# Performance work log

Hardware: AMD Instinct MI355X
Metric: run time of the kernel (lower is better)

The kernel has to match this reference:

```python
import jax, jax.numpy as jnp
import numpy as np

N_NODES = 100000
N_EDGES = 1250000
IN_C, HID_C, OUT_C = 64, 128, 64


def setup_inputs() -> dict:
    key = jax.random.key(0)
    ks = jax.random.split(key, 9)
    x = jax.random.normal(ks[0], (N_NODES, IN_C), dtype=jnp.float32)
    edge_index = jax.random.randint(ks[1], (2, N_EDGES), 0, N_NODES, dtype=jnp.int64)
    s = 0.1
    return {
        "x": x,
        "edge_index": edge_index,
        "W_l0": jax.random.normal(ks[2], (IN_C, HID_C), dtype=jnp.float32) * s,
        "W_r0": jax.random.normal(ks[3], (IN_C, HID_C), dtype=jnp.float32) * s,
        "b_l0": jnp.zeros((HID_C,), dtype=jnp.float32),
        "W_l1": jax.random.normal(ks[4], (HID_C, HID_C), dtype=jnp.float32) * s,
        "W_r1": jax.random.normal(ks[5], (HID_C, HID_C), dtype=jnp.float32) * s,
        "b_l1": jnp.zeros((HID_C,), dtype=jnp.float32),
        "W_out": jax.random.normal(ks[6], (HID_C, OUT_C), dtype=jnp.float32) * s,
        "b_out": jnp.zeros((OUT_C,), dtype=jnp.float32),
    }


def _sage_conv(x, src, dst, W_l, b_l, W_r):
    # mean-aggregate source features onto destination nodes
    agg = jax.ops.segment_sum(x[src], dst, num_segments=N_NODES)  # [N, d]
    deg = jax.ops.segment_sum(jnp.ones((src.shape[0],), x.dtype), dst,
                              num_segments=N_NODES)
    mean = agg / jnp.maximum(deg, 1.0)[:, None]
    # out = lin_l(mean_neighbors) + lin_r(x_self); bias only on lin_l (PyG)
    return mean @ W_l + b_l + x @ W_r


def reference(x, edge_index, W_l0, W_r0, b_l0, W_l1, W_r1, b_l1, W_out, b_out):
    src, dst = edge_index[0], edge_index[1]
    h = jax.nn.relu(_sage_conv(x, src, dst, W_l0, b_l0, W_r0))  # dropout = identity (eval)
    h = jax.nn.relu(_sage_conv(h, src, dst, W_l1, b_l1, W_r1))
    return h @ W_out + b_out
```

## Files before the change

### kernel.cpp

```cpp
#include <hip/hip_runtime.h>

#define N_NODES 100000
#define N_EDGES 1250000
#define IN_C 64
#define HID_C 128
#define OUT_C 64
#define NBUCK 98
#define BCAP 16384
#define PA_EPT 16
#define PA_EPB (256 * PA_EPT)
#define PA_BLOCKS ((N_EDGES + PA_EPB - 1) / PA_EPB)
#define BB_EPT 16

typedef __attribute__((ext_vector_type(8))) short short8;
typedef __attribute__((ext_vector_type(4))) float f32x4;

__device__ __forceinline__ float bflo(unsigned u) { return __uint_as_float(u << 16); }
__device__ __forceinline__ float bfhi(unsigned u) { return __uint_as_float(u & 0xffff0000u); }
__device__ __forceinline__ unsigned short f2bf(float f) {
    unsigned u = __float_as_uint(f);
    return (unsigned short)((u + 0x7fffu + ((u >> 16) & 1u)) >> 16);
}
__device__ __forceinline__ unsigned packbf(float lo, float hi) {
    return ((unsigned)f2bf(hi) << 16) | f2bf(lo);
}
__device__ __forceinline__ void acc8(const uint4 u, float* a) {
    a[0] += bflo(u.x); a[1] += bfhi(u.x);
    a[2] += bflo(u.y); a[3] += bfhi(u.y);
    a[4] += bflo(u.z); a[5] += bfhi(u.z);
    a[6] += bflo(u.w); a[7] += bfhi(u.w);
}

#define GLOBAL_AS __attribute__((address_space(1)))
#define LDS_AS __attribute__((address_space(3)))
__device__ __forceinline__ void load_lds16(const void* g, void* l) {
    __builtin_amdgcn_global_load_lds((const GLOBAL_AS void*)g, (LDS_AS void*)l, 16, 0, 0);
}

__global__ void detect_i64_kernel(const unsigned int* __restrict__ e, int* __restrict__ flag) {
    unsigned v = e[2 * threadIdx.x + 1];
    unsigned long long b = __ballot(v != 0u);
    if (threadIdx.x == 0) flag[0] = (b == 0ull) ? 1 : 0;
}

__global__ __launch_bounds__(256) void bucketize_kernel(const unsigned int* __restrict__ e,
                                                        const int* __restrict__ flag,
                                                        int* __restrict__ bucketCount,
                                                        unsigned* __restrict__ pairs) {
    __shared__ int cnt[NBUCK];
    __shared__ int base[NBUCK];
    const bool i64 = flag[0] != 0;
    for (int t = threadIdx.x; t < NBUCK; t += 256) cnt[t] = 0;
    __syncthreads();
    const int e0 = blockIdx.x * PA_EPB;
    unsigned s[PA_EPT], d[PA_EPT];
    int rank[PA_EPT];
#pragma unroll
    for (int j = 0; j < PA_EPT; ++j) {
        int i = e0 + j * 256 + threadIdx.x;
        if (i < N_EDGES) {
            s[j] = i64 ? e[2 * i] : e[i];
            d[j] = i64 ? e[2 * (N_EDGES + i)] : e[N_EDGES + i];
            rank[j] = atomicAdd(&cnt[d[j] >> 10], 1);
        }
    }
    __syncthreads();
    for (int t = threadIdx.x; t < NBUCK; t += 256)
        base[t] = atomicAdd(&bucketCount[t], cnt[t]);
    __syncthreads();
#pragma unroll
    for (int j = 0; j < PA_EPT; ++j) {
        int i = e0 + j * 256 + threadIdx.x;
        if (i < N_EDGES) {
            unsigned b = d[j] >> 10;
            pairs[b * BCAP + base[b] + rank[j]] = s[j] | ((d[j] & 1023u) << 17);
        }
    }
}

__global__ void bucket_scan_kernel(const int* __restrict__ bucketCount,
                                   int* __restrict__ bucketBase, int* __restrict__ csr_off) {
    __shared__ int s[128];
    int tid = threadIdx.x;
    int v = (tid < NBUCK) ? bucketCount[tid] : 0;
    s[tid] = v;
    __syncthreads();
    for (int off = 1; off < 128; off <<= 1) {
        int t = (tid >= off) ? s[tid - off] : 0;
        __syncthreads();
        s[tid] += t;
        __syncthreads();
    }
    if (tid < NBUCK) bucketBase[tid] = s[tid] - v;
    if (tid == 0) csr_off[N_NODES] = N_EDGES;
}

__global__ __launch_bounds__(1024) void bucket_build_kernel(
    const unsigned* __restrict__ pairs, const int* __restrict__ bucketCount,
    const int* __restrict__ bucketBase, int* __restrict__ csr_off, int* __restrict__ csr_src) {
    __shared__ int deg[1024];
    __shared__ int sc[1024];
    const int k = blockIdx.x;
    const int tid = threadIdx.x;
    const int count = bucketCount[k];
    const int gbase = bucketBase[k];
    deg[tid] = 0;
    __syncthreads();
    unsigned sp[BB_EPT];
    int rk[BB_EPT];
#pragma unroll
    for (int j = 0; j < BB_EPT; ++j) {
        int idx = j * 1024 + tid;
        if (idx < count) {
            unsigned u = pairs[(size_t)k * BCAP + idx];
            sp[j] = u;
            rk[j] = atomicAdd(&deg[u >> 17], 1);
        }
    }
    __syncthreads();
    const int own = deg[tid];
    sc[tid] = own;
    __syncthreads();
    for (int off = 1; off < 1024; off <<= 1) {
        int t = (tid >= off) ? sc[tid - off] : 0;
        __syncthreads();
        sc[tid] += t;
        __syncthreads();
    }
    const int excl = sc[tid] - own;
    const int node = k * 1024 + tid;
    if (node < N_NODES) csr_off[node] = gbase + excl;
    __syncthreads();
    deg[tid] = excl;
    __syncthreads();
#pragma unroll
    for (int j = 0; j < BB_EPT; ++j) {
        int idx = j * 1024 + tid;
        if (idx < count) {
            unsigned ld = sp[j] >> 17;
            csr_src[gbase + deg[ld] + rk[j]] = (int)(sp[j] & 0x1FFFFu);
        }
    }
}

__global__ void cvt_x_kernel(const float* __restrict__ x, unsigned short* __restrict__ xb) {
    int i = blockIdx.x * blockDim.x + threadIdx.x;
    if (i >= N_NODES * IN_C / 4) return;
    float4 v = ((const float4*)x)[i];
    unsigned lo = ((unsigned)f2bf(v.y) << 16) | f2bf(v.x);
    unsigned hi = ((unsigned)f2bf(v.w) << 16) | f2bf(v.z);
    ((uint2*)xb)[i] = make_uint2(lo, hi);
}

__global__ void cvt_w_kernel(const float* __restrict__ Wl0, const float* __restrict__ Wr0,
                             const float* __restrict__ Wl1, const float* __restrict__ Wr1,
                             const float* __restrict__ Wo, unsigned short* __restrict__ wb) {
    int i = blockIdx.x * blockDim.x + threadIdx.x;
    if (i >= 57344) return;
    float v;
    if (i < 8192) {
        int col = i >> 6, k = i & 63;
        v = Wl0[k * HID_C + col];
    } else if (i < 16384) {
        int j = i - 8192;
        int col = j >> 6, k = j & 63;
        v = Wr0[k * HID_C + col];
    } else if (i < 32768) {
        int j = i - 16384;
        int col = j >> 7, k = j & 127;
        v = Wl1[k * HID_C + col];
    } else if (i < 49152) {
        int j = i - 32768;
        int col = j >> 7, k = j & 127;
        v = Wr1[k * HID_C + col];
    } else {
        int j = i - 49152;
        int col = j >> 7, k = j & 127;
        v = Wo[k * OUT_C + col];
    }
    wb[i] = f2bf(v);
}

__global__ __launch_bounds__(256) void agg0_kernel(
    const unsigned short* __restrict__ xb, const int* __restrict__ off,
    const int* __restrict__ csr_src, unsigned short* __restrict__ mean0b) {
    int wid = (blockIdx.x * 256 + threadIdx.x) >> 6;
    int lane = threadIdx.x & 63;
    if (wid >= N_NODES) return;
    const int slot = lane >> 3;
    const int c4 = lane & 7;
    int beg = off[wid], end = off[wid + 1];
    const uint4* base = (const uint4*)xb;
    float a[8] = {0.f, 0.f, 0.f, 0.f, 0.f, 0.f, 0.f, 0.f};
    int e = beg + slot;
    for (; e + 8 < end; e += 16) {
        uint4 ua = base[(size_t)csr_src[e] * 8 + c4];
        uint4 ub = base[(size_t)csr_src[e + 8] * 8 + c4];
        acc8(ua, a);
        acc8(ub, a);
    }
    if (e < end) acc8(base[(size_t)csr_src[e] * 8 + c4], a);
#pragma unroll
    for (int j = 0; j < 8; ++j) {
        a[j] += __shfl_xor(a[j], 8);
        a[j] += __shfl_xor(a[j], 16);
        a[j] += __shfl_xor(a[j], 32);
    }
    if (slot == 0) {
        float invd = (end > beg) ? 1.f / (float)(end - beg) : 0.f;
        uint4 o;
        o.x = packbf(a[0] * invd, a[1] * invd);
        o.y = packbf(a[2] * invd, a[3] * invd);
        o.z = packbf(a[4] * invd, a[5] * invd);
        o.w = packbf(a[6] * invd, a[7] * invd);
        ((uint4*)mean0b)[(size_t)wid * 8 + c4] = o;
    }
}

__global__ __launch_bounds__(256) void agg1_kernel(
    const unsigned short* __restrict__ h0b, const int* __restrict__ off,
    const int* __restrict__ csr_src, unsigned short* __restrict__ mean1b) {
    int wid = (blockIdx.x * 256 + threadIdx.x) >> 6;
    int lane = threadIdx.x & 63;
    if (wid >= N_NODES) return;
    const int slot = lane >> 4;
    const int c4 = lane & 15;
    int beg = off[wid], end = off[wid + 1];
    const uint4* base = (const uint4*)h0b;
    float a[8] = {0.f, 0.f, 0.f, 0.f, 0.f, 0.f, 0.f, 0.f};
    int e = beg + slot;
    for (; e + 4 < end; e += 8) {
        uint4 ua = base[(size_t)csr_src[e] * 16 + c4];
        uint4 ub = base[(size_t)csr_src[e + 4] * 16 + c4];
        acc8(ua, a);
        acc8(ub, a);
    }
    if (e < end) acc8(base[(size_t)csr_src[e] * 16 + c4], a);
#pragma unroll
    for (int j = 0; j < 8; ++j) {
        a[j] += __shfl_xor(a[j], 16);
        a[j] += __shfl_xor(a[j], 32);
    }
    if (slot == 0) {
        float invd = (end > beg) ? 1.f / (float)(end - beg) : 0.f;
        uint4 o;
        o.x = packbf(a[0] * invd, a[1] * invd);
        o.y = packbf(a[2] * invd, a[3] * invd);
        o.z = packbf(a[4] * invd, a[5] * invd);
        o.w = packbf(a[6] * invd, a[7] * invd);
        ((uint4*)mean1b)[(size_t)wid * 16 + c4] = o;
    }
}

__global__ __launch_bounds__(512) void gemm0_kernel(
    const unsigned short* __restrict__ mean0b, const unsigned short* __restrict__ xb,
    const unsigned short* __restrict__ WlT, const unsigned short* __restrict__ WrT,
    const float* __restrict__ b0, unsigned short* __restrict__ h0b) {
    __shared__ unsigned short sa[64 * IN_C];
    __shared__ unsigned short sh[64 * IN_C];
    const int wave = threadIdx.x >> 6, lane = threadIdx.x & 63;
    const int r16 = lane & 15, q = lane >> 4;
    const int col = wave * 16 + r16;
    const int node0 = blockIdx.x * 64;

    {
        int t = threadIdx.x;
        int row = t >> 3, seg = t & 7;
        int grow = node0 + row;
        if (grow >= N_NODES) grow = N_NODES - 1;
        size_t soff = (size_t)grow * IN_C + (size_t)((seg ^ (row & 7)) * 8);
        load_lds16(mean0b + soff, sa + t * 8);
        load_lds16(xb + soff, sh + t * 8);
    }

    short8 bl[2], br[2];
#pragma unroll
    for (int s = 0; s < 2; ++s) {
        bl[s] = *(const short8*)(WlT + col * IN_C + s * 32 + q * 8);
        br[s] = *(const short8*)(WrT + col * IN_C + s * 32 + q * 8);
    }
    const float bias = b0[col];

    asm volatile("s_waitcnt vmcnt(0)" ::: "memory");
    __syncthreads();

#pragma unroll
    for (int r = 0; r < 4; ++r) {
        const int lrow = r * 16 + r16;
        const int rsw = lrow & 7;
        short8 am[2], ax[2];
#pragma unroll
        for (int s = 0; s < 2; ++s) {
            int seg = s * 4 + q;
            int off = lrow * IN_C + ((seg ^ rsw) * 8);
            am[s] = *(const short8*)(sa + off);
            ax[s] = *(const short8*)(sh + off);
        }
        f32x4 accA, accB;
        accA[0] = bias; accA[1] = bias; accA[2] = bias; accA[3] = bias;
        accB[0] = 0.f; accB[1] = 0.f; accB[2] = 0.f; accB[3] = 0.f;
#pragma unroll
        for (int s = 0; s < 2; ++s) {
            accA = __builtin_amdgcn_mfma_f32_16x16x32_bf16(am[s], bl[s], accA, 0, 0, 0);
            accB = __builtin_amdgcn_mfma_f32_16x16x32_bf16(ax[s], br[s], accB, 0, 0, 0);
        }
#pragma unroll
        for (int rr = 0; rr < 4; ++rr) {
            int row = node0 + r * 16 + q * 4 + rr;
            if (row < N_NODES)
                h0b[(size_t)row * HID_C + col] = f2bf(fmaxf(accA[rr] + accB[rr], 0.f));
        }
    }
}

__global__ __launch_bounds__(512) void gemm1_kernel(
    const unsigned short* __restrict__ mean1b, const unsigned short* __restrict__ h0b,
    const unsigned short* __restrict__ WlT, const unsigned short* __restrict__ WrT,
    const unsigned short* __restrict__ WoT, const float* __restrict__ b1,
    const float* __restrict__ bo, float* __restrict__ out) {
    __shared__ unsigned short sa[64 * HID_C];
    __shared__ unsigned short sh[64 * HID_C];
    __shared__ unsigned short h1s[64 * HID_C];
    const int wave = threadIdx.x >> 6, lane = threadIdx.x & 63;
    const int r16 = lane & 15, q = lane >> 4;
    const int col = wave * 16 + r16;
    const int node0 = blockIdx.x * 64;

    {
        int t = threadIdx.x;
#pragma unroll
        for (int c = 0; c < 4; ++c) {
            int idx = (c & 1) * 512 + t;
            int row = idx >> 4, seg = idx & 15;
            int grow = node0 + row;
            if (grow >= N_NODES) grow = N_NODES - 1;
            size_t soff = (size_t)grow * HID_C + (size_t)((seg ^ (row & 7)) * 8);
            if (c < 2) load_lds16(mean1b + soff, sa + idx * 8);
            else load_lds16(h0b + soff, sh + idx * 8);
        }
    }

    short8 bw0[4], bw1[4], wo[4];
    const int ct = wave & 3;
    const int wcol = ct * 16 + r16;
#pragma unroll
    for (int s = 0; s < 4; ++s) {
        bw0[s] = *(const short8*)(WlT + col * HID_C + s * 32 + q * 8);
        bw1[s] = *(const short8*)(WrT + col * HID_C + s * 32 + q * 8);
        wo[s] = *(const short8*)(WoT + wcol * HID_C + s * 32 + q * 8);
    }
    const float bias1 = b1[col];
    const float biaso = bo[wcol];

    asm volatile("s_waitcnt vmcnt(0)" ::: "memory");
    __syncthreads();

#pragma unroll
    for (int r = 0; r < 4; ++r) {
        const int lrow = r * 16 + r16;
        const int rsw = lrow & 7;
        short8 am[4], ah[4];
#pragma unroll
        for (int s = 0; s < 4; ++s) {
            int seg = s * 4 + q;
            int off = lrow * HID_C + ((seg ^ rsw) * 8);
            am[s] = *(const short8*)(sa + off);
            ah[s] = *(const short8*)(sh + off);
        }
        f32x4 accA, accB;
        accA[0] = bias1; accA[1] = bias1; accA[2] = bias1; accA[3] = bias1;
        accB[0] = 0.f; accB[1] = 0.f; accB[2] = 0.f; accB[3] = 0.f;
#pragma unroll
        for (int s = 0; s < 4; ++s) {
            accA = __builtin_amdgcn_mfma_f32_16x16x32_bf16(am[s], bw0[s], accA, 0, 0, 0);
            accB = __builtin_amdgcn_mfma_f32_16x16x32_bf16(ah[s], bw1[s], accB, 0, 0, 0);
        }
#pragma unroll
        for (int rr = 0; rr < 4; ++rr) {
            int ar = r * 16 + q * 4 + rr;
            int off = (ar * 256 + col * 2) ^ ((ar & 7) << 4);
            *(unsigned short*)((char*)h1s + off) = f2bf(fmaxf(accA[rr] + accB[rr], 0.f));
        }
    }
    __syncthreads();

#pragma unroll
    for (int t = 0; t < 2; ++t) {
        const int rs = (wave >> 2) + 2 * t;
        f32x4 oa;
        oa[0] = biaso; oa[1] = biaso; oa[2] = biaso; oa[3] = biaso;
#pragma unroll
        for (int s = 0; s < 4; ++s) {
            int ar = rs * 16 + r16;
            int off = (ar * 256 + (s * 32 + q * 8) * 2) ^ ((ar & 7) << 4);
            short8 a = *(const short8*)((const char*)h1s + off);
            oa = __builtin_amdgcn_mfma_f32_16x16x32_bf16(a, wo[s], oa, 0, 0, 0);
        }
#pragma unroll
        for (int rr = 0; rr < 4; ++rr) {
            int row = node0 + rs * 16 + q * 4 + rr;
            if (row < N_NODES) out[(size_t)row * OUT_C + wcol] = oa[rr];
        }
    }
}

extern "C" void kernel_launch(void* const* d_in, const int* in_sizes, int n_in,
                              void* d_out, int out_size, void* d_ws, size_t ws_size,
                              hipStream_t stream) {
    const float* x = (const float*)d_in[0];
    const unsigned int* edge = (const unsigned int*)d_in[1];
    const float* Wl0 = (const float*)d_in[2];
    const float* Wr0 = (const float*)d_in[3];
    const float* bl0 = (const float*)d_in[4];
    const float* Wl1 = (const float*)d_in[5];
    const float* Wr1 = (const float*)d_in[6];
    const float* bl1 = (const float*)d_in[7];
    const float* Wo = (const float*)d_in[8];
    const float* bo = (const float*)d_in[9];
    float* out = (float*)d_out;

    char* w = (char*)d_ws;
    auto alloc = [&](size_t bytes) {
        char* p = w;
        w += (bytes + 255) & ~(size_t)255;
        return p;
    };
    int* flag = (int*)alloc(256);
    int* bucketCount = (int*)alloc(NBUCK * 4);
    int* bucketBase = (int*)alloc(NBUCK * 4);
    int* csr_off = (int*)alloc((size_t)(N_NODES + 1) * 4);
    int* csr_src = (int*)alloc((size_t)N_EDGES * 4);
    unsigned* pairs = (unsigned*)alloc((size_t)NBUCK * BCAP * 4);
    unsigned short* xb = (unsigned short*)alloc((size_t)N_NODES * IN_C * 2);
    unsigned short* mean0b = (unsigned short*)alloc((size_t)N_NODES * IN_C * 2);
    unsigned short* h0b = (unsigned short*)alloc((size_t)N_NODES * HID_C * 2);
    unsigned short* mean1b = (unsigned short*)alloc((size_t)N_NODES * HID_C * 2);
    unsigned short* wb = (unsigned short*)alloc(57344 * 2);

    const unsigned short* Wl0T = wb;
    const unsigned short* Wr0T = wb + 8192;
    const unsigned short* Wl1T = wb + 16384;
    const unsigned short* Wr1T = wb + 32768;
    const unsigned short* WoT = wb + 49152;

    hipMemsetAsync(bucketCount, 0, NBUCK * 4, stream);
    detect_i64_kernel<<<1, 64, 0, stream>>>(edge, flag);
    bucketize_kernel<<<PA_BLOCKS, 256, 0, stream>>>(edge, flag, bucketCount, pairs);
    bucket_scan_kernel<<<1, 128, 0, stream>>>(bucketCount, bucketBase, csr_off);
    bucket_build_kernel<<<NBUCK, 1024, 0, stream>>>(pairs, bucketCount, bucketBase, csr_off,
                                                    csr_src);

    cvt_x_kernel<<<(N_NODES * IN_C / 4 + 255) / 256, 256, 0, stream>>>(x, xb);
    cvt_w_kernel<<<(57344 + 255) / 256, 256, 0, stream>>>(Wl0, Wr0, Wl1, Wr1, Wo, wb);

    const int AGG_BLOCKS = (N_NODES * 64 + 255) / 256;
    const int GEMM_BLOCKS = (N_NODES + 63) / 64;

    agg0_kernel<<<AGG_BLOCKS, 256, 0, stream>>>(xb, csr_off, csr_src, mean0b);
    gemm0_kernel<<<GEMM_BLOCKS, 512, 0, stream>>>(mean0b, xb, Wl0T, Wr0T, bl0, h0b);
    agg1_kernel<<<AGG_BLOCKS, 256, 0, stream>>>(h0b, csr_off, csr_src, mean1b);
    gemm1_kernel<<<GEMM_BLOCKS, 512, 0, stream>>>(mean1b, h0b, Wl1T, Wr1T, WoT, bl1, bo, out);
}
```

Measured before the change: 184.6 us.

## Fold small setup kernels into neighbours and process four nodes per aggregation wave

Removes the dtype-detect, bucket-scan and separate weight-convert launches by folding their work into bucketize, bucket_build and a merged convert kernel, cutting launch count. Each aggregation wave now handles four nodes in sequence instead of one, and accumulators use float2 vectors so the compiler can emit packed adds. In exchange, every bucket_build block recomputes the 98-entry scan redundantly, and the aggregation kernels launch fewer waves, which may reduce latency hiding on the gathers.

```diff
diff --git a/kernel.cpp b/kernel.cpp
--- a/kernel.cpp
+++ b/kernel.cpp
@@ -14,6 +14,7 @@
 
 typedef __attribute__((ext_vector_type(8))) short short8;
 typedef __attribute__((ext_vector_type(4))) float f32x4;
+typedef __attribute__((ext_vector_type(2))) float f32x2;
 
 __device__ __forceinline__ float bflo(unsigned u) { return __uint_as_float(u << 16); }
 __device__ __forceinline__ float bfhi(unsigned u) { return __uint_as_float(u & 0xffff0000u); }
@@ -24,11 +25,17 @@
 __device__ __forceinline__ unsigned packbf(float lo, float hi) {
     return ((unsigned)f2bf(hi) << 16) | f2bf(lo);
 }
-__device__ __forceinline__ void acc8(const uint4 u, float* a) {
-    a[0] += bflo(u.x); a[1] += bfhi(u.x);
-    a[2] += bflo(u.y); a[3] += bfhi(u.y);
-    a[4] += bflo(u.z); a[5] += bfhi(u.z);
-    a[6] += bflo(u.w); a[7] += bfhi(u.w);
+__device__ __forceinline__ f32x2 up2(unsigned u) {
+    f32x2 r;
+    r[0] = bflo(u);
+    r[1] = bfhi(u);
+    return r;
+}
+__device__ __forceinline__ void acc8p(const uint4 u, f32x2* a) {
+    a[0] += up2(u.x);
+    a[1] += up2(u.y);
+    a[2] += up2(u.z);
+    a[3] += up2(u.w);
 }
 
 #define GLOBAL_AS __attribute__((address_space(1)))
@@ -37,21 +44,20 @@
     __builtin_amdgcn_global_load_lds((const GLOBAL_AS void*)g, (LDS_AS void*)l, 16, 0, 0);
 }
 
-__global__ void detect_i64_kernel(const unsigned int* __restrict__ e, int* __restrict__ flag) {
-    unsigned v = e[2 * threadIdx.x + 1];
-    unsigned long long b = __ballot(v != 0u);
-    if (threadIdx.x == 0) flag[0] = (b == 0ull) ? 1 : 0;
-}
-
 __global__ __launch_bounds__(256) void bucketize_kernel(const unsigned int* __restrict__ e,
-                                                        const int* __restrict__ flag,
                                                         int* __restrict__ bucketCount,
                                                         unsigned* __restrict__ pairs) {
     __shared__ int cnt[NBUCK];
     __shared__ int base[NBUCK];
-    const bool i64 = flag[0] != 0;
+    __shared__ int flag_s;
+    {
+        unsigned v = e[2 * (threadIdx.x & 63) + 1];
+        unsigned long long b = __ballot(v != 0u);
+        if (threadIdx.x == 0) flag_s = (b == 0ull) ? 1 : 0;
+    }
     for (int t = threadIdx.x; t < NBUCK; t += 256) cnt[t] = 0;
     __syncthreads();
+    const bool i64 = flag_s != 0;
     const int e0 = blockIdx.x * PA_EPB;
     unsigned s[PA_EPT], d[PA_EPT];
     int rank[PA_EPT];
@@ -78,34 +84,27 @@
     }
 }
 
-__global__ void bucket_scan_kernel(const int* __restrict__ bucketCount,
-                                   int* __restrict__ bucketBase, int* __restrict__ csr_off) {
-    __shared__ int s[128];
-    int tid = threadIdx.x;
-    int v = (tid < NBUCK) ? bucketCount[tid] : 0;
-    s[tid] = v;
-    __syncthreads();
-    for (int off = 1; off < 128; off <<= 1) {
-        int t = (tid >= off) ? s[tid - off] : 0;
-        __syncthreads();
-        s[tid] += t;
-        __syncthreads();
-    }
-    if (tid < NBUCK) bucketBase[tid] = s[tid] - v;
-    if (tid == 0) csr_off[N_NODES] = N_EDGES;
-}
-
 __global__ __launch_bounds__(1024) void bucket_build_kernel(
     const unsigned* __restrict__ pairs, const int* __restrict__ bucketCount,
-    const int* __restrict__ bucketBase, int* __restrict__ csr_off, int* __restrict__ csr_src) {
+    int* __restrict__ csr_off, int* __restrict__ csr_src) {
     __shared__ int deg[1024];
     __shared__ int sc[1024];
+    __shared__ int bc[128];
     const int k = blockIdx.x;
     const int tid = threadIdx.x;
+    if (tid < 128) bc[tid] = (tid < NBUCK) ? bucketCount[tid] : 0;
+    deg[tid] = 0;
+    __syncthreads();
+    for (int off = 1; off < 128; off <<= 1) {
+        int t = (tid >= off && tid < 128) ? bc[tid - off] : 0;
+        __syncthreads();
+        if (tid < 128) bc[tid] += t;
+        __syncthreads();
+    }
     const int count = bucketCount[k];
-    const int gbase = bucketBase[k];
-    deg[tid] = 0;
-    __syncthreads();
+    const int gbase = bc[k] - count;
+    if (k == 0 && tid == 0) csr_off[N_NODES] = N_EDGES;
+
     unsigned sp[BB_EPT];
     int rk[BB_EPT];
 #pragma unroll
@@ -143,112 +142,126 @@
     }
 }
 
-__global__ void cvt_x_kernel(const float* __restrict__ x, unsigned short* __restrict__ xb) {
+#define CVT_X_N (N_NODES * IN_C / 4)
+__global__ void cvt_kernel(const float* __restrict__ x, unsigned short* __restrict__ xb,
+                           const float* __restrict__ Wl0, const float* __restrict__ Wr0,
+                           const float* __restrict__ Wl1, const float* __restrict__ Wr1,
+                           const float* __restrict__ Wo, unsigned short* __restrict__ wb) {
     int i = blockIdx.x * blockDim.x + threadIdx.x;
-    if (i >= N_NODES * IN_C / 4) return;
-    float4 v = ((const float4*)x)[i];
-    unsigned lo = ((unsigned)f2bf(v.y) << 16) | f2bf(v.x);
-    unsigned hi = ((unsigned)f2bf(v.w) << 16) | f2bf(v.z);
-    ((uint2*)xb)[i] = make_uint2(lo, hi);
-}
-
-__global__ void cvt_w_kernel(const float* __restrict__ Wl0, const float* __restrict__ Wr0,
-                             const float* __restrict__ Wl1, const float* __restrict__ Wr1,
-                             const float* __restrict__ Wo, unsigned short* __restrict__ wb) {
-    int i = blockIdx.x * blockDim.x + threadIdx.x;
-    if (i >= 57344) return;
+    if (i < CVT_X_N) {
+        float4 v = ((const float4*)x)[i];
+        unsigned lo = ((unsigned)f2bf(v.y) << 16) | f2bf(v.x);
+        unsigned hi = ((unsigned)f2bf(v.w) << 16) | f2bf(v.z);
+        ((uint2*)xb)[i] = make_uint2(lo, hi);
+        return;
+    }
+    int j = i - CVT_X_N;
+    if (j >= 57344) return;
     float v;
-    if (i < 8192) {
-        int col = i >> 6, k = i & 63;
+    if (j < 8192) {
+        int col = j >> 6, k = j & 63;
         v = Wl0[k * HID_C + col];
-    } else if (i < 16384) {
-        int j = i - 8192;
-        int col = j >> 6, k = j & 63;
+    } else if (j < 16384) {
+        int jj = j - 8192;
+        int col = jj >> 6, k = jj & 63;
         v = Wr0[k * HID_C + col];
-    } else if (i < 32768) {
-        int j = i - 16384;
-        int col = j >> 7, k = j & 127;
+    } else if (j < 32768) {
+        int jj = j - 16384;
+        int col = jj >> 7, k = jj & 127;
         v = Wl1[k * HID_C + col];
-    } else if (i < 49152) {
-        int j = i - 32768;
-        int col = j >> 7, k = j & 127;
+    } else if (j < 49152) {
+        int jj = j - 32768;
+        int col = jj >> 7, k = jj & 127;
         v = Wr1[k * HID_C + col];
     } else {
-        int j = i - 49152;
-        int col = j >> 7, k = j & 127;
+        int jj = j - 49152;
+        int col = jj >> 7, k = jj & 127;
         v = Wo[k * OUT_C + col];
     }
-    wb[i] = f2bf(v);
+    wb[j] = f2bf(v);
 }
 
 __global__ __launch_bounds__(256) void agg0_kernel(
     const unsigned short* __restrict__ xb, const int* __restrict__ off,
     const int* __restrict__ csr_src, unsigned short* __restrict__ mean0b) {
-    int wid = (blockIdx.x * 256 + threadIdx.x) >> 6;
-    int lane = threadIdx.x & 63;
-    if (wid >= N_NODES) return;
+    const int wave = (blockIdx.x * 256 + threadIdx.x) >> 6;
+    const int lane = threadIdx.x & 63;
     const int slot = lane >> 3;
     const int c4 = lane & 7;
-    int beg = off[wid], end = off[wid + 1];
     const uint4* base = (const uint4*)xb;
-    float a[8] = {0.f, 0.f, 0.f, 0.f, 0.f, 0.f, 0.f, 0.f};
-    int e = beg + slot;
-    for (; e + 8 < end; e += 16) {
-        uint4 ua = base[(size_t)csr_src[e] * 8 + c4];
-        uint4 ub = base[(size_t)csr_src[e + 8] * 8 + c4];
-        acc8(ua, a);
-        acc8(ub, a);
-    }
-    if (e < end) acc8(base[(size_t)csr_src[e] * 8 + c4], a);
-#pragma unroll
-    for (int j = 0; j < 8; ++j) {
-        a[j] += __shfl_xor(a[j], 8);
-        a[j] += __shfl_xor(a[j], 16);
-        a[j] += __shfl_xor(a[j], 32);
-    }
-    if (slot == 0) {
-        float invd = (end > beg) ? 1.f / (float)(end - beg) : 0.f;
-        uint4 o;
-        o.x = packbf(a[0] * invd, a[1] * invd);
-        o.y = packbf(a[2] * invd, a[3] * invd);
-        o.z = packbf(a[4] * invd, a[5] * invd);
-        o.w = packbf(a[6] * invd, a[7] * invd);
-        ((uint4*)mean0b)[(size_t)wid * 8 + c4] = o;
+#pragma unroll
+    for (int n = 0; n < 4; ++n) {
+        const int wid = wave * 4 + n;
+        if (wid >= N_NODES) return;
+        int beg = off[wid], end = off[wid + 1];
+        f32x2 a[4] = {{0.f, 0.f}, {0.f, 0.f}, {0.f, 0.f}, {0.f, 0.f}};
+        int e = beg + slot;
+        for (; e + 8 < end; e += 16) {
+            uint4 ua = base[(size_t)csr_src[e] * 8 + c4];
+            uint4 ub = base[(size_t)csr_src[e + 8] * 8 + c4];
+            acc8p(ua, a);
+            acc8p(ub, a);
+        }
+        if (e < end) acc8p(base[(size_t)csr_src[e] * 8 + c4], a);
+#pragma unroll
+        for (int j = 0; j < 4; ++j) {
+            a[j][0] += __shfl_xor(a[j][0], 8);
+            a[j][1] += __shfl_xor(a[j][1], 8);
+            a[j][0] += __shfl_xor(a[j][0], 16);
+            a[j][1] += __shfl_xor(a[j][1], 16);
+            a[j][0] += __shfl_xor(a[j][0], 32);
+            a[j][1] += __shfl_xor(a[j][1], 32);
+        }
+        if (slot == 0) {
+            float invd = (end > beg) ? 1.f / (float)(end - beg) : 0.f;
+            uint4 o;
+            o.x = packbf(a[0][0] * invd, a[0][1] * invd);
+            o.y = packbf(a[1][0] * invd, a[1][1] * invd);
+            o.z = packbf(a[2][0] * invd, a[2][1] * invd);
+            o.w = packbf(a[3][0] * invd, a[3][1] * invd);
+            ((uint4*)mean0b)[(size_t)wid * 8 + c4] = o;
+        }
     }
 }
 
 __global__ __launch_bounds__(256) void agg1_kernel(
     const unsigned short* __restrict__ h0b, const int* __restrict__ off,
     const int* __restrict__ csr_src, unsigned short* __restrict__ mean1b) {
-    int wid = (blockIdx.x * 256 + threadIdx.x) >> 6;
-    int lane = threadIdx.x & 63;
-    if (wid >= N_NODES) return;
+    const int wave = (blockIdx.x * 256 + threadIdx.x) >> 6;
+    const int lane = threadIdx.x & 63;
     const int slot = lane >> 4;
     const int c4 = lane & 15;
-    int beg = off[wid], end = off[wid + 1];
     const uint4* base = (const uint4*)h0b;
-    float a[8] = {0.f, 0.f, 0.f, 0.f, 0.f, 0.f, 0.f, 0.f};
-    int e = beg + slot;
-    for (; e + 4 < end; e += 8) {
-        uint4 ua = base[(size_t)csr_src[e] * 16 + c4];
-        uint4 ub = base[(size_t)csr_src[e + 4] * 16 + c4];
-        acc8(ua, a);
-        acc8(ub, a);
-    }
-    if (e < end) acc8(base[(size_t)csr_src[e] * 16 + c4], a);
-#pragma unroll
-    for (int j = 0; j < 8; ++j) {
-        a[j] += __shfl_xor(a[j], 16);
-        a[j] += __shfl_xor(a[j], 32);
-    }
-    if (slot == 0) {
-        float invd = (end > beg) ? 1.f / (float)(end - beg) : 0.f;
-        uint4 o;
-        o.x = packbf(a[0] * invd, a[1] * invd);
-        o.y = packbf(a[2] * invd, a[3] * invd);
-        o.z = packbf(a[4] * invd, a[5] * invd);
-        o.w = packbf(a[6] * invd, a[7] * invd);
-        ((uint4*)mean1b)[(size_t)wid * 16 + c4] = o;
+#pragma unroll
+    for (int n = 0; n < 4; ++n) {
+        const int wid = wave * 4 + n;
+        if (wid >= N_NODES) return;
+        int beg = off[wid], end = off[wid + 1];
+        f32x2 a[4] = {{0.f, 0.f}, {0.f, 0.f}, {0.f, 0.f}, {0.f, 0.f}};
+        int e = beg + slot;
+        for (; e + 4 < end; e += 8) {
+            uint4 ua = base[(size_t)csr_src[e] * 16 + c4];
+            uint4 ub = base[(size_t)csr_src[e + 4] * 16 + c4];
+            acc8p(ua, a);
+            acc8p(ub, a);
+        }
+        if (e < end) acc8p(base[(size_t)csr_src[e] * 16 + c4], a);
+#pragma unroll
+        for (int j = 0; j < 4; ++j) {
+            a[j][0] += __shfl_xor(a[j][0], 16);
+            a[j][1] += __shfl_xor(a[j][1], 16);
+            a[j][0] += __shfl_xor(a[j][0], 32);
+            a[j][1] += __shfl_xor(a[j][1], 32);
+        }
+        if (slot == 0) {
+            float invd = (end > beg) ? 1.f / (float)(end - beg) : 0.f;
+            uint4 o;
+            o.x = packbf(a[0][0] * invd, a[0][1] * invd);
+            o.y = packbf(a[1][0] * invd, a[1][1] * invd);
+            o.z = packbf(a[2][0] * invd, a[2][1] * invd);
+            o.w = packbf(a[3][0] * invd, a[3][1] * invd);
+            ((uint4*)mean1b)[(size_t)wid * 16 + c4] = o;
+        }
     }
 }
 
@@ -425,9 +438,7 @@
         w += (bytes + 255) & ~(size_t)255;
         return p;
     };
-    int* flag = (int*)alloc(256);
     int* bucketCount = (int*)alloc(NBUCK * 4);
-    int* bucketBase = (int*)alloc(NBUCK * 4);
     int* csr_off = (int*)alloc((size_t)(N_NODES + 1) * 4);
     int* csr_src = (int*)alloc((size_t)N_EDGES * 4);
     unsigned* pairs = (unsigned*)alloc((size_t)NBUCK * BCAP * 4);
@@ -444,16 +455,13 @@
     const unsigned short* WoT = wb + 49152;
 
     hipMemsetAsync(bucketCount, 0, NBUCK * 4, stream);
-    detect_i64_kernel<<<1, 64, 0, stream>>>(edge, flag);
-    bucketize_kernel<<<PA_BLOCKS, 256, 0, stream>>>(edge, flag, bucketCount, pairs);
-    bucket_scan_kernel<<<1, 128, 0, stream>>>(bucketCount, bucketBase, csr_off);
-    bucket_build_kernel<<<NBUCK, 1024, 0, stream>>>(pairs, bucketCount, bucketBase, csr_off,
-                                                    csr_src);
-
-    cvt_x_kernel<<<(N_NODES * IN_C / 4 + 255) / 256, 256, 0, stream>>>(x, xb);
-    cvt_w_kernel<<<(57344 + 255) / 256, 256, 0, stream>>>(Wl0, Wr0, Wl1, Wr1, Wo, wb);
-
-    const int AGG_BLOCKS = (N_NODES * 64 + 255) / 256;
+    bucketize_kernel<<<PA_BLOCKS, 256, 0, stream>>>(edge, bucketCount, pairs);
+    bucket_build_kernel<<<NBUCK, 1024, 0, stream>>>(pairs, bucketCount, csr_off, csr_src);
+
+    cvt_kernel<<<(CVT_X_N + 57344 + 255) / 256, 256, 0, stream>>>(x, xb, Wl0, Wr0, Wl1, Wr1,
+                                                                  Wo, wb);
+
+    const int AGG_BLOCKS = (N_NODES + 15) / 16;
     const int GEMM_BLOCKS = (N_NODES + 63) / 64;
 
     agg0_kernel<<<AGG_BLOCKS, 256, 0, stream>>>(xb, csr_off, csr_src, mean0b);
```

After: 181.9 us. About the same (-1.4%).
